# Performance work log

Hardware: AMD Instinct MI355X
Metric: run time of the kernel (lower is better)

Reference implementation:

```python
import jax, jax.numpy as jnp
import numpy as np

N0, N1, N2, N3 = 200000, 50000, 12000, 3000
E0, E1, E2 = 500000, 120000, 30000
D_IN, D_H, D_OUT = 256, 256, 64


def setup_inputs() -> dict:
    key = jax.random.key(0)
    ks = jax.random.split(key, 16)
    s = 1.0 / np.sqrt(D_IN)
    return {
        "x": jax.random.normal(ks[0], (N0, D_IN), jnp.float32),
        "src0": jax.random.randint(ks[1], (E0,), 0, N0),
        "dst0": jax.random.randint(ks[2], (E0,), 0, N1),
        "src1": jax.random.randint(ks[3], (E1,), 0, N1),
        "dst1": jax.random.randint(ks[4], (E1,), 0, N2),
        "src2": jax.random.randint(ks[5], (E2,), 0, N2),
        "dst2": jax.random.randint(ks[6], (E2,), 0, N3),
        "num_dst0": N1, "num_dst1": N2, "num_dst2": N3,
        "Ws0": jax.random.normal(ks[7], (D_IN, D_H), jnp.float32) * s,
        "Wn0": jax.random.normal(ks[8], (D_IN, D_H), jnp.float32) * s,
        "b0": jnp.zeros((D_H,), jnp.float32),
        "Ws1": jax.random.normal(ks[9], (D_H, D_H), jnp.float32) * s,
        "Wn1": jax.random.normal(ks[10], (D_H, D_H), jnp.float32) * s,
        "b1": jnp.zeros((D_H,), jnp.float32),
        "Ws2": jax.random.normal(ks[11], (D_H, D_OUT), jnp.float32) * s,
        "Wn2": jax.random.normal(ks[12], (D_H, D_OUT), jnp.float32) * s,
        "b2": jnp.zeros((D_OUT,), jnp.float32),
    }


def sage_conv(src, dst, num_dst, h_src, Wn, Ws, b):
    # DGL SAGEConv(mean): fc_self(h_dst) + fc_neigh(mean_{in-edges} h_src) + bias
    h_dst = h_src[:num_dst]
    msg = h_src[src]                                          # [E, d] gather
    agg = jax.ops.segment_sum(msg, dst, num_segments=num_dst)  # [num_dst, d]
    deg = jax.ops.segment_sum(jnp.ones((dst.shape[0],), h_src.dtype), dst,
                              num_segments=num_dst)
    h_neigh = agg / jnp.maximum(deg, 1.0)[:, None]
    return h_dst @ Ws + h_neigh @ Wn + b


def reference(x, src0, dst0, src1, dst1, src2, dst2,
              num_dst0, num_dst1, num_dst2,
              Ws0, Wn0, b0, Ws1, Wn1, b1, Ws2, Wn2, b2):
    h = sage_conv(src0, dst0, num_dst0, x, Wn0, Ws0, b0)       # layer 0 (no act, per source)
    h = sage_conv(src1, dst1, num_dst1, h, Wn1, Ws1, b1)       # layer 1
    h = jax.nn.relu(h)                                         # activation after middle layer
    # dropout omitted (eval / deterministic mode)
    h = sage_conv(src2, dst2, num_dst2, h, Wn2, Ws2, b2)       # layer 2
    return h
```

## Files before the change

### kernel.cpp

```cpp
#include <hip/hip_runtime.h>

#define N0_SRC 200000
#define N1_DST 50000
#define N2_DST 12000
#define N3_DST 3000
#define NTOT_DST 65000
#define DH 256
#define DOUT 64
#define EMAX_TOT 650000

#define CONV_BLOCKS 6250
#define TRANS_BLOCKS 1536
#define ZERO_BLOCKS 254

typedef __attribute__((ext_vector_type(8))) short short8;
typedef __attribute__((ext_vector_type(4))) float f32x4;

__device__ __forceinline__ ushort f2bf(float f) {
    union { float f; uint32_t u; } v; v.f = f;
    uint32_t r = (v.u + 0x7FFF + ((v.u >> 16) & 1)) >> 16;
    return (ushort)r;
}
__device__ __forceinline__ float bf2f(ushort u) {
    union { uint32_t u; float f; } v; v.u = ((uint32_t)u) << 16;
    return v.f;
}

__device__ __forceinline__ void gload16(const ushort* g, ushort* l) {
    __builtin_amdgcn_global_load_lds(
        (const __attribute__((address_space(1))) unsigned int*)g,
        (__attribute__((address_space(3))) unsigned int*)l,
        16, 0, 0);
}

__global__ void prep_kernel(const float* __restrict__ x,
                            const float* __restrict__ W0, const float* __restrict__ W1,
                            const float* __restrict__ W2, const float* __restrict__ W3,
                            const float* __restrict__ W4, const float* __restrict__ W5,
                            ushort* __restrict__ Wt, int* __restrict__ cnt,
                            ushort* __restrict__ xb50) {
    int bid = blockIdx.x;
    if (bid < CONV_BLOCKS) {
        long i = ((long)bid * 256 + threadIdx.x) * 8;
        float4 a = *(const float4*)(x + i);
        float4 b = *(const float4*)(x + i + 4);
        ushort4 o0, o1;
        o0.x = f2bf(a.x); o0.y = f2bf(a.y); o0.z = f2bf(a.z); o0.w = f2bf(a.w);
        o1.x = f2bf(b.x); o1.y = f2bf(b.y); o1.z = f2bf(b.z); o1.w = f2bf(b.w);
        *(ushort4*)(xb50 + i) = o0;
        *(ushort4*)(xb50 + i + 4) = o1;
        return;
    }
    if (bid < CONV_BLOCKS + TRANS_BLOCKS) {
        int tb = bid - CONV_BLOCKS;
        int wy = tb >> 8;
        int wx = tb & 255;
        const float* W; int Ndim; ushort* o;
        switch (wy) {
            case 0: W = W0; Ndim = 256; o = Wt; break;
            case 1: W = W1; Ndim = 256; o = Wt + 65536; break;
            case 2: W = W2; Ndim = 256; o = Wt + 131072; break;
            case 3: W = W3; Ndim = 256; o = Wt + 196608; break;
            case 4: W = W4; Ndim = 64;  o = Wt + 262144; break;
            default: W = W5; Ndim = 64; o = Wt + 278528; break;
        }
        int id = wx * 256 + threadIdx.x;
        int n = id >> 8;
        int k = id & 255;
        if (n >= Ndim) return;
        o[id] = f2bf(W[k * Ndim + n]);
        return;
    }
    int z = (bid - CONV_BLOCKS - TRANS_BLOCKS) * 256 + threadIdx.x;
    if (z < NTOT_DST) cnt[z] = 0;
}

__global__ void hist3_kernel(const int* __restrict__ d0, int E0,
                             const int* __restrict__ d1, int E1,
                             const int* __restrict__ d2, int E2,
                             int* __restrict__ cnt) {
    int layer = blockIdx.y;
    const int* dst; int E; int base;
    if (layer == 0)      { dst = d0; E = E0; base = 0; }
    else if (layer == 1) { dst = d1; E = E1; base = N1_DST; }
    else                 { dst = d2; E = E2; base = N1_DST + N2_DST; }
    int e = blockIdx.x * 256 + threadIdx.x;
    if (e < E) atomicAdd(&cnt[base + dst[e]], 1);
}

__global__ void fill3_kernel(const int* __restrict__ s0, const int* __restrict__ d0, int E0,
                             const int* __restrict__ s1, const int* __restrict__ d1, int E1,
                             const int* __restrict__ s2, const int* __restrict__ d2, int E2,
                             int* __restrict__ cursor, int* __restrict__ eidx) {
    int layer = blockIdx.y;
    const int* src; const int* dst; int E; int base;
    if (layer == 0)      { src = s0; dst = d0; E = E0; base = 0; }
    else if (layer == 1) { src = s1; dst = d1; E = E1; base = N1_DST; }
    else                 { src = s2; dst = d2; E = E2; base = N1_DST + N2_DST; }
    int e = blockIdx.x * 256 + threadIdx.x;
    if (e < E) {
        int p = atomicAdd(&cursor[base + dst[e]], 1);
        eidx[p] = src[e];
    }
}

__global__ void scan_phase_a(const int* __restrict__ cnt, int* __restrict__ partial, int n) {
    __shared__ int red[4];
    int t = threadIdx.x;
    int i = blockIdx.x * 1024 + t * 4;
    int s = 0;
    if (i + 3 < n) {
        int4 v = *(const int4*)(cnt + i);
        s = v.x + v.y + v.z + v.w;
    }
#pragma unroll
    for (int d = 32; d; d >>= 1) s += __shfl_down(s, d, 64);
    if ((t & 63) == 0) red[t >> 6] = s;
    __syncthreads();
    if (t == 0) partial[blockIdx.x] = red[0] + red[1] + red[2] + red[3];
}

__global__ void scan_phase_c(const int* __restrict__ cnt, const int* __restrict__ partial,
                             int* __restrict__ off, int* __restrict__ cursor, int n) {
    __shared__ int tsum[256];
    __shared__ int pbase;
    int t = threadIdx.x;
    if (t < 64) {
        int own = partial[t];
        int v = own;
#pragma unroll
        for (int d = 1; d < 64; d <<= 1) {
            int u = __shfl_up(v, d, 64);
            if (t >= d) v += u;
        }
        if (t == blockIdx.x) pbase = v - own;
    }
    int i = blockIdx.x * 1024 + t * 4;
    int4 c = make_int4(0, 0, 0, 0);
    if (i + 3 < n) c = *(const int4*)(cnt + i);
    int s = c.x + c.y + c.z + c.w;
    tsum[t] = s;
    __syncthreads();
#pragma unroll
    for (int d = 1; d < 256; d <<= 1) {
        int u = (t >= d) ? tsum[t - d] : 0;
        __syncthreads();
        tsum[t] += u;
        __syncthreads();
    }
    int base = pbase + tsum[t] - s;
    if (i + 3 < n) {
        int4 ov;
        ov.x = base;
        ov.y = ov.x + c.x;
        ov.z = ov.y + c.y;
        ov.w = ov.z + c.z;
        *(int4*)(off + i) = ov;
        *(int4*)(cursor + i) = ov;
        if (i + 4 == n) off[n] = ov.w + c.w;
    }
}

__global__ void gather_mean_f32_kernel(const float* __restrict__ h,
                                       const int* __restrict__ off,
                                       const int* __restrict__ eidx,
                                       ushort* __restrict__ hn,
                                       int num_dst) {
    int w = blockIdx.x * 4 + (threadIdx.x >> 6);
    int lane = threadIdx.x & 63;
    if (w >= num_dst) return;
    int beg = off[w];
    int end = off[w + 1];
    float a0 = 0.f, a1 = 0.f, a2 = 0.f, a3 = 0.f;
    for (int i = beg; i < end; i += 4) {
        int rem = end - i;
        int j1 = i + (rem > 1 ? 1 : 0);
        int j2 = i + (rem > 2 ? 2 : 0);
        int j3 = i + (rem > 3 ? 3 : 0);
        float m1 = rem > 1 ? 1.f : 0.f;
        float m2 = rem > 2 ? 1.f : 0.f;
        float m3 = rem > 3 ? 1.f : 0.f;
        int s0 = eidx[i], s1 = eidx[j1], s2 = eidx[j2], s3 = eidx[j3];
        float4 v0 = ((const float4*)(h + (size_t)s0 * DH))[lane];
        float4 v1 = ((const float4*)(h + (size_t)s1 * DH))[lane];
        float4 v2 = ((const float4*)(h + (size_t)s2 * DH))[lane];
        float4 v3 = ((const float4*)(h + (size_t)s3 * DH))[lane];
        a0 += v0.x + m1 * v1.x + m2 * v2.x + m3 * v3.x;
        a1 += v0.y + m1 * v1.y + m2 * v2.y + m3 * v3.y;
        a2 += v0.z + m1 * v1.z + m2 * v2.z + m3 * v3.z;
        a3 += v0.w + m1 * v1.w + m2 * v2.w + m3 * v3.w;
    }
    float inv = 1.0f / fmaxf((float)(end - beg), 1.0f);
    ushort4 o;
    o.x = f2bf(a0 * inv); o.y = f2bf(a1 * inv);
    o.z = f2bf(a2 * inv); o.w = f2bf(a3 * inv);
    *(ushort4*)(hn + (size_t)w * DH + lane * 4) = o;
}

__global__ void gather_mean_bf16_kernel(const ushort* __restrict__ h,
                                        const int* __restrict__ off,
                                        const int* __restrict__ eidx,
                                        ushort* __restrict__ hn,
                                        int num_dst) {
    int w = blockIdx.x * 4 + (threadIdx.x >> 6);
    int lane = threadIdx.x & 63;
    if (w >= num_dst) return;
    int beg = off[w];
    int end = off[w + 1];
    float a0 = 0.f, a1 = 0.f, a2 = 0.f, a3 = 0.f;
    for (int i = beg; i < end; i += 4) {
        int rem = end - i;
        int j1 = i + (rem > 1 ? 1 : 0);
        int j2 = i + (rem > 2 ? 2 : 0);
        int j3 = i + (rem > 3 ? 3 : 0);
        float m1 = rem > 1 ? 1.f : 0.f;
        float m2 = rem > 2 ? 1.f : 0.f;
        float m3 = rem > 3 ? 1.f : 0.f;
        int s0 = eidx[i], s1 = eidx[j1], s2 = eidx[j2], s3 = eidx[j3];
        ushort4 v0 = ((const ushort4*)(h + (size_t)s0 * DH))[lane];
        ushort4 v1 = ((const ushort4*)(h + (size_t)s1 * DH))[lane];
        ushort4 v2 = ((const ushort4*)(h + (size_t)s2 * DH))[lane];
        ushort4 v3 = ((const ushort4*)(h + (size_t)s3 * DH))[lane];
        a0 += bf2f(v0.x) + m1 * bf2f(v1.x) + m2 * bf2f(v2.x) + m3 * bf2f(v3.x);
        a1 += bf2f(v0.y) + m1 * bf2f(v1.y) + m2 * bf2f(v2.y) + m3 * bf2f(v3.y);
        a2 += bf2f(v0.z) + m1 * bf2f(v1.z) + m2 * bf2f(v2.z) + m3 * bf2f(v3.z);
        a3 += bf2f(v0.w) + m1 * bf2f(v1.w) + m2 * bf2f(v2.w) + m3 * bf2f(v3.w);
    }
    float inv = 1.0f / fmaxf((float)(end - beg), 1.0f);
    ushort4 o;
    o.x = f2bf(a0 * inv); o.y = f2bf(a1 * inv);
    o.z = f2bf(a2 * inv); o.w = f2bf(a3 * inv);
    *(ushort4*)(hn + (size_t)w * DH + lane * 4) = o;
}

template <int MT, int NT, bool RELU, bool OUT_BF16>
__global__ __launch_bounds__(256) void gemm_dual(const ushort* __restrict__ Ad,
                                                 const ushort* __restrict__ An,
                                                 const ushort* __restrict__ Wst,
                                                 const ushort* __restrict__ Wnt,
                                                 const float* __restrict__ bias,
                                                 void* __restrict__ Cv,
                                                 int M, int N) {
    const int K = 256;
    const int BM = MT * 64;
    const int BN = NT * 16;
    __shared__ __align__(16) ushort lds[(2 * BM + 2 * BN) * 32];
    ushort* Asd = lds;
    ushort* Asn = lds + BM * 32;
    ushort* Bss = lds + 2 * BM * 32;
    ushort* Bsn = lds + 2 * BM * 32 + BN * 32;

    int tid  = threadIdx.x;
    int lane = tid & 63;
    int wid  = tid >> 6;
    int q    = lane >> 4;
    int mr   = lane & 15;
    int row0 = blockIdx.y * BM;
    int col0 = blockIdx.x * BN;

    f32x4 acc[MT][NT];
#pragma unroll
    for (int i = 0; i < MT; ++i)
#pragma unroll
        for (int j = 0; j < NT; ++j) acc[i][j] = (f32x4){0.f, 0.f, 0.f, 0.f};

    for (int k0 = 0; k0 < K; k0 += 32) {
#pragma unroll
        for (int c = 0; c < MT; ++c) {
            int chunk = c * 256 + tid;
            int r   = chunk >> 2;
            int sg  = (chunk & 3) ^ ((r >> 1) & 3);
            int row = row0 + r;
            if (row > M - 1) row = M - 1;
            const ushort* gd = Ad + (size_t)row * K + k0 + sg * 8;
            const ushort* gn = An + (size_t)row * K + k0 + sg * 8;
            int cb = (c * 256 + (tid & ~63)) * 8;
            gload16(gd, Asd + cb);
            gload16(gn, Asn + cb);
        }
#pragma unroll
        for (int c = 0; c < NT / 4; ++c) {
            int chunk = c * 256 + tid;
            int r  = chunk >> 2;
            int sg = (chunk & 3) ^ ((r >> 1) & 3);
            const ushort* gs = Wst + (size_t)(col0 + r) * K + k0 + sg * 8;
            const ushort* gw = Wnt + (size_t)(col0 + r) * K + k0 + sg * 8;
            int cb = (c * 256 + (tid & ~63)) * 8;
            gload16(gs, Bss + cb);
            gload16(gw, Bsn + cb);
        }
        __syncthreads();

        short8 ad[MT], an[MT];
#pragma unroll
        for (int mt = 0; mt < MT; ++mt) {
            int rho = wid * (MT * 16) + mt * 16 + mr;
            int o   = rho * 32 + ((q ^ ((rho >> 1) & 3)) * 8);
            ad[mt] = *(const short8*)(Asd + o);
            an[mt] = *(const short8*)(Asn + o);
        }
#pragma unroll
        for (int nt = 0; nt < NT; ++nt) {
            int rho = nt * 16 + mr;
            int o   = rho * 32 + ((q ^ ((rho >> 1) & 3)) * 8);
            short8 bs = *(const short8*)(Bss + o);
            short8 bn = *(const short8*)(Bsn + o);
#pragma unroll
            for (int mt = 0; mt < MT; ++mt)
                acc[mt][nt] = __builtin_amdgcn_mfma_f32_16x16x32_bf16(
                    ad[mt], bs, acc[mt][nt], 0, 0, 0);
#pragma unroll
            for (int mt = 0; mt < MT; ++mt)
                acc[mt][nt] = __builtin_amdgcn_mfma_f32_16x16x32_bf16(
                    an[mt], bn, acc[mt][nt], 0, 0, 0);
        }
        __syncthreads();
    }

#pragma unroll
    for (int mt = 0; mt < MT; ++mt) {
#pragma unroll
        for (int i = 0; i < 4; ++i) {
            int row = row0 + wid * (MT * 16) + mt * 16 + q * 4 + i;
            if (row >= M) continue;
#pragma unroll
            for (int nt = 0; nt < NT; ++nt) {
                int col = col0 + nt * 16 + mr;
                float v = acc[mt][nt][i] + bias[col];
                if (RELU) v = fmaxf(v, 0.0f);
                if (OUT_BF16) ((ushort*)Cv)[(size_t)row * N + col] = f2bf(v);
                else          ((float*)Cv)[(size_t)row * N + col] = v;
            }
        }
    }
}

extern "C" void kernel_launch(void* const* d_in, const int* in_sizes, int n_in,
                              void* d_out, int out_size, void* d_ws, size_t ws_size,
                              hipStream_t stream) {
    const float* x    = (const float*)d_in[0];
    const int* src0   = (const int*)d_in[1];
    const int* dst0   = (const int*)d_in[2];
    const int* src1   = (const int*)d_in[3];
    const int* dst1   = (const int*)d_in[4];
    const int* src2   = (const int*)d_in[5];
    const int* dst2   = (const int*)d_in[6];
    const float* Ws0  = (const float*)d_in[10];
    const float* Wn0  = (const float*)d_in[11];
    const float* b0   = (const float*)d_in[12];
    const float* Ws1  = (const float*)d_in[13];
    const float* Wn1  = (const float*)d_in[14];
    const float* b1   = (const float*)d_in[15];
    const float* Ws2  = (const float*)d_in[16];
    const float* Wn2  = (const float*)d_in[17];
    const float* b2   = (const float*)d_in[18];
    float* out = (float*)d_out;

    int E0 = in_sizes[1];
    int E1 = in_sizes[3];
    int E2 = in_sizes[5];

    ushort* wsu  = (ushort*)d_ws;
    ushort* xb50 = wsu;
    ushort* hn0b = xb50 + (size_t)N1_DST * DH;
    ushort* h1b  = hn0b + (size_t)N1_DST * DH;
    ushort* hn1b = h1b  + (size_t)N1_DST * DH;
    ushort* h2b  = hn1b + (size_t)N2_DST * DH;
    ushort* hn2b = h2b  + (size_t)N2_DST * DH;
    ushort* Wt   = hn2b + (size_t)N3_DST * DH;
    ushort* Ws0t = Wt;
    ushort* Wn0t = Wt + 65536;
    ushort* Ws1t = Wt + 131072;
    ushort* Wn1t = Wt + 196608;
    ushort* Ws2t = Wt + 262144;
    ushort* Wn2t = Wt + 278528;
    int* cnt     = (int*)(Wt + 294912);
    int* off     = cnt + NTOT_DST;
    int* cursor  = off + NTOT_DST + 4;
    int* eidx    = cursor + NTOT_DST;
    int* partial = eidx + EMAX_TOT;

    prep_kernel<<<CONV_BLOCKS + TRANS_BLOCKS + ZERO_BLOCKS, 256, 0, stream>>>(
        x, Ws0, Wn0, Ws1, Wn1, Ws2, Wn2, Wt, cnt, xb50);

    int Emax = max(max(E0, E1), E2);
    int nb = (NTOT_DST + 1023) / 1024;
    hist3_kernel<<<dim3((Emax + 255) / 256, 3), 256, 0, stream>>>(dst0, E0, dst1, E1, dst2, E2, cnt);
    scan_phase_a<<<nb, 256, 0, stream>>>(cnt, partial, NTOT_DST);
    scan_phase_c<<<nb, 256, 0, stream>>>(cnt, partial, off, cursor, NTOT_DST);
    fill3_kernel<<<dim3((Emax + 255) / 256, 3), 256, 0, stream>>>(
        src0, dst0, E0, src1, dst1, E1, src2, dst2, E2, cursor, eidx);

    const int* off0 = off;
    const int* off1 = off + N1_DST;
    const int* off2 = off + N1_DST + N2_DST;

    gather_mean_f32_kernel<<<(N1_DST + 3) / 4, 256, 0, stream>>>(x, off0, eidx, hn0b, N1_DST);
    gemm_dual<2, 16, false, true><<<dim3(1, (N1_DST + 127) / 128), 256, 0, stream>>>(
        xb50, hn0b, Ws0t, Wn0t, b0, h1b, N1_DST, DH);

    gather_mean_bf16_kernel<<<(N2_DST + 3) / 4, 256, 0, stream>>>(h1b, off1, eidx, hn1b, N2_DST);
    gemm_dual<2, 16, true, true><<<dim3(1, (N2_DST + 127) / 128), 256, 0, stream>>>(
        h1b, hn1b, Ws1t, Wn1t, b1, h2b, N2_DST, DH);

    gather_mean_bf16_kernel<<<(N3_DST + 3) / 4, 256, 0, stream>>>(h2b, off2, eidx, hn2b, N3_DST);
    gemm_dual<1, 4, false, false><<<dim3(DOUT / 64, (N3_DST + 63) / 64), 256, 0, stream>>>(
        h2b, hn2b, Ws2t, Wn2t, b2, out, N3_DST, DOUT);
}
```

Measured before the change: 507.5 us.

## Fuse CSR prep into cooperative kernel, unroll gathers by eight, split GEMM tiles

The separate prep, histogram, two scan phases and fill launches become one cooperative kernel that uses grid-wide syncs between phases, which removes four launch gaps. The gather-mean kernels now issue eight row loads per iteration instead of four, giving more memory-level parallelism per wave. The layer 0 and 1 GEMMs use a 128-wide N tile over two grid columns, doubling the block count. Risks: grid.sync costs, a fixed 2048-block grid that must fit co-resident on the device, and more registers in the gather kernels.

New measurement: 1.353 ms. +166.6%, slower.

```diff
diff --git a/kernel.cpp b/kernel.cpp
--- a/kernel.cpp
+++ b/kernel.cpp
@@ -1,4 +1,7 @@
 #include <hip/hip_runtime.h>
+#include <hip/hip_cooperative_groups.h>
+
+namespace cg = cooperative_groups;
 
 #define N0_SRC 200000
 #define N1_DST 50000
@@ -9,9 +12,7 @@
 #define DOUT 64
 #define EMAX_TOT 650000
 
-#define CONV_BLOCKS 6250
-#define TRANS_BLOCKS 1536
-#define ZERO_BLOCKS 254
+#define PREP_BLOCKS 2048
 
 typedef __attribute__((ext_vector_type(8))) short short8;
 typedef __attribute__((ext_vector_type(4))) float f32x4;
@@ -33,132 +34,107 @@
         16, 0, 0);
 }
 
-__global__ void prep_kernel(const float* __restrict__ x,
-                            const float* __restrict__ W0, const float* __restrict__ W1,
-                            const float* __restrict__ W2, const float* __restrict__ W3,
-                            const float* __restrict__ W4, const float* __restrict__ W5,
-                            ushort* __restrict__ Wt, int* __restrict__ cnt,
-                            ushort* __restrict__ xb50) {
-    int bid = blockIdx.x;
-    if (bid < CONV_BLOCKS) {
-        long i = ((long)bid * 256 + threadIdx.x) * 8;
-        float4 a = *(const float4*)(x + i);
-        float4 b = *(const float4*)(x + i + 4);
-        ushort4 o0, o1;
-        o0.x = f2bf(a.x); o0.y = f2bf(a.y); o0.z = f2bf(a.z); o0.w = f2bf(a.w);
-        o1.x = f2bf(b.x); o1.y = f2bf(b.y); o1.z = f2bf(b.z); o1.w = f2bf(b.w);
-        *(ushort4*)(xb50 + i) = o0;
-        *(ushort4*)(xb50 + i + 4) = o1;
-        return;
-    }
-    if (bid < CONV_BLOCKS + TRANS_BLOCKS) {
-        int tb = bid - CONV_BLOCKS;
-        int wy = tb >> 8;
-        int wx = tb & 255;
-        const float* W; int Ndim; ushort* o;
-        switch (wy) {
-            case 0: W = W0; Ndim = 256; o = Wt; break;
-            case 1: W = W1; Ndim = 256; o = Wt + 65536; break;
-            case 2: W = W2; Ndim = 256; o = Wt + 131072; break;
-            case 3: W = W3; Ndim = 256; o = Wt + 196608; break;
-            case 4: W = W4; Ndim = 64;  o = Wt + 262144; break;
-            default: W = W5; Ndim = 64; o = Wt + 278528; break;
-        }
-        int id = wx * 256 + threadIdx.x;
-        int n = id >> 8;
-        int k = id & 255;
-        if (n >= Ndim) return;
-        o[id] = f2bf(W[k * Ndim + n]);
-        return;
-    }
-    int z = (bid - CONV_BLOCKS - TRANS_BLOCKS) * 256 + threadIdx.x;
-    if (z < NTOT_DST) cnt[z] = 0;
-}
-
-__global__ void hist3_kernel(const int* __restrict__ d0, int E0,
-                             const int* __restrict__ d1, int E1,
-                             const int* __restrict__ d2, int E2,
-                             int* __restrict__ cnt) {
-    int layer = blockIdx.y;
-    const int* dst; int E; int base;
-    if (layer == 0)      { dst = d0; E = E0; base = 0; }
-    else if (layer == 1) { dst = d1; E = E1; base = N1_DST; }
-    else                 { dst = d2; E = E2; base = N1_DST + N2_DST; }
-    int e = blockIdx.x * 256 + threadIdx.x;
-    if (e < E) atomicAdd(&cnt[base + dst[e]], 1);
-}
-
-__global__ void fill3_kernel(const int* __restrict__ s0, const int* __restrict__ d0, int E0,
-                             const int* __restrict__ s1, const int* __restrict__ d1, int E1,
-                             const int* __restrict__ s2, const int* __restrict__ d2, int E2,
-                             int* __restrict__ cursor, int* __restrict__ eidx) {
-    int layer = blockIdx.y;
-    const int* src; const int* dst; int E; int base;
-    if (layer == 0)      { src = s0; dst = d0; E = E0; base = 0; }
-    else if (layer == 1) { src = s1; dst = d1; E = E1; base = N1_DST; }
-    else                 { src = s2; dst = d2; E = E2; base = N1_DST + N2_DST; }
-    int e = blockIdx.x * 256 + threadIdx.x;
-    if (e < E) {
-        int p = atomicAdd(&cursor[base + dst[e]], 1);
-        eidx[p] = src[e];
-    }
-}
-
-__global__ void scan_phase_a(const int* __restrict__ cnt, int* __restrict__ partial, int n) {
+struct PrepArgs {
+    const float* x;
+    const float* W[6];
+    const int* s0; const int* d0; int E0;
+    const int* s1; const int* d1; int E1;
+    const int* s2; const int* d2; int E2;
+    ushort* Wt; ushort* xb50;
+    int* cnt; int* off; int* cursor; int* eidx; int* partial;
+};
+
+__global__ __launch_bounds__(256) void prep_csr_kernel(PrepArgs a) {
+    cg::grid_group grid = cg::this_grid();
     __shared__ int red[4];
-    int t = threadIdx.x;
-    int i = blockIdx.x * 1024 + t * 4;
-    int s = 0;
-    if (i + 3 < n) {
-        int4 v = *(const int4*)(cnt + i);
-        s = v.x + v.y + v.z + v.w;
-    }
-#pragma unroll
-    for (int d = 32; d; d >>= 1) s += __shfl_down(s, d, 64);
-    if ((t & 63) == 0) red[t >> 6] = s;
-    __syncthreads();
-    if (t == 0) partial[blockIdx.x] = red[0] + red[1] + red[2] + red[3];
-}
-
-__global__ void scan_phase_c(const int* __restrict__ cnt, const int* __restrict__ partial,
-                             int* __restrict__ off, int* __restrict__ cursor, int n) {
     __shared__ int tsum[256];
     __shared__ int pbase;
-    int t = threadIdx.x;
-    if (t < 64) {
-        int own = partial[t];
-        int v = own;
-#pragma unroll
-        for (int d = 1; d < 64; d <<= 1) {
-            int u = __shfl_up(v, d, 64);
-            if (t >= d) v += u;
-        }
-        if (t == blockIdx.x) pbase = v - own;
-    }
-    int i = blockIdx.x * 1024 + t * 4;
-    int4 c = make_int4(0, 0, 0, 0);
-    if (i + 3 < n) c = *(const int4*)(cnt + i);
-    int s = c.x + c.y + c.z + c.w;
-    tsum[t] = s;
-    __syncthreads();
-#pragma unroll
-    for (int d = 1; d < 256; d <<= 1) {
-        int u = (t >= d) ? tsum[t - d] : 0;
+    const int GT = PREP_BLOCKS * 256;
+    int gt = blockIdx.x * 256 + threadIdx.x;
+    int t  = threadIdx.x;
+
+    for (int i = gt; i < NTOT_DST; i += GT) a.cnt[i] = 0;
+    {
+        const float4* xv = (const float4*)a.x;
+        ushort4* xo = (ushort4*)a.xb50;
+        const int nv = N1_DST * DH / 4;
+        for (int i = gt; i < nv; i += GT) {
+            float4 v = xv[i];
+            ushort4 o;
+            o.x = f2bf(v.x); o.y = f2bf(v.y); o.z = f2bf(v.z); o.w = f2bf(v.w);
+            xo[i] = o;
+        }
+    }
+    for (int i = gt; i < 294912; i += GT) {
+        const float* W; ushort* o; int id; int Ndim;
+        if (i < 262144) { int wy = i >> 16; id = i & 65535; W = a.W[wy]; o = a.Wt + (wy << 16); Ndim = 256; }
+        else { int j = i - 262144; int wy = j >> 14; id = j & 16383; W = a.W[4 + wy]; o = a.Wt + 262144 + (wy << 14); Ndim = 64; }
+        int n = id >> 8, k = id & 255;
+        o[id] = f2bf(W[k * Ndim + n]);
+    }
+    grid.sync();
+
+    for (int e = gt; e < a.E0; e += GT) atomicAdd(&a.cnt[a.d0[e]], 1);
+    for (int e = gt; e < a.E1; e += GT) atomicAdd(&a.cnt[N1_DST + a.d1[e]], 1);
+    for (int e = gt; e < a.E2; e += GT) atomicAdd(&a.cnt[N1_DST + N2_DST + a.d2[e]], 1);
+    grid.sync();
+
+    if (blockIdx.x < 64) {
+        int i = blockIdx.x * 1024 + t * 4;
+        int s = 0;
+        if (i + 3 < NTOT_DST) {
+            int4 v = *(const int4*)(a.cnt + i);
+            s = v.x + v.y + v.z + v.w;
+        }
+#pragma unroll
+        for (int d = 32; d; d >>= 1) s += __shfl_down(s, d, 64);
+        if ((t & 63) == 0) red[t >> 6] = s;
         __syncthreads();
-        tsum[t] += u;
+        if (t == 0) a.partial[blockIdx.x] = red[0] + red[1] + red[2] + red[3];
+    }
+    grid.sync();
+
+    if (blockIdx.x < 64) {
+        if (t < 64) {
+            int own = a.partial[t];
+            int v = own;
+#pragma unroll
+            for (int d = 1; d < 64; d <<= 1) {
+                int u = __shfl_up(v, d, 64);
+                if (t >= d) v += u;
+            }
+            if (t == (int)blockIdx.x) pbase = v - own;
+        }
+        int i = blockIdx.x * 1024 + t * 4;
+        int4 c = make_int4(0, 0, 0, 0);
+        if (i + 3 < NTOT_DST) c = *(const int4*)(a.cnt + i);
+        int s = c.x + c.y + c.z + c.w;
+        tsum[t] = s;
         __syncthreads();
-    }
-    int base = pbase + tsum[t] - s;
-    if (i + 3 < n) {
-        int4 ov;
-        ov.x = base;
-        ov.y = ov.x + c.x;
-        ov.z = ov.y + c.y;
-        ov.w = ov.z + c.z;
-        *(int4*)(off + i) = ov;
-        *(int4*)(cursor + i) = ov;
-        if (i + 4 == n) off[n] = ov.w + c.w;
-    }
+#pragma unroll
+        for (int d = 1; d < 256; d <<= 1) {
+            int u = (t >= d) ? tsum[t - d] : 0;
+            __syncthreads();
+            tsum[t] += u;
+            __syncthreads();
+        }
+        int base = pbase + tsum[t] - s;
+        if (i + 3 < NTOT_DST) {
+            int4 ov;
+            ov.x = base;
+            ov.y = ov.x + c.x;
+            ov.z = ov.y + c.y;
+            ov.w = ov.z + c.z;
+            *(int4*)(a.off + i) = ov;
+            *(int4*)(a.cursor + i) = ov;
+            if (i + 4 == NTOT_DST) a.off[NTOT_DST] = ov.w + c.w;
+        }
+    }
+    grid.sync();
+
+    for (int e = gt; e < a.E0; e += GT) { int p = atomicAdd(&a.cursor[a.d0[e]], 1); a.eidx[p] = a.s0[e]; }
+    for (int e = gt; e < a.E1; e += GT) { int p = atomicAdd(&a.cursor[N1_DST + a.d1[e]], 1); a.eidx[p] = a.s1[e]; }
+    for (int e = gt; e < a.E2; e += GT) { int p = atomicAdd(&a.cursor[N1_DST + N2_DST + a.d2[e]], 1); a.eidx[p] = a.s2[e]; }
 }
 
 __global__ void gather_mean_f32_kernel(const float* __restrict__ h,
@@ -172,23 +148,40 @@
     int beg = off[w];
     int end = off[w + 1];
     float a0 = 0.f, a1 = 0.f, a2 = 0.f, a3 = 0.f;
-    for (int i = beg; i < end; i += 4) {
+    for (int i = beg; i < end; i += 8) {
         int rem = end - i;
         int j1 = i + (rem > 1 ? 1 : 0);
         int j2 = i + (rem > 2 ? 2 : 0);
         int j3 = i + (rem > 3 ? 3 : 0);
+        int j4 = i + (rem > 4 ? 4 : 0);
+        int j5 = i + (rem > 5 ? 5 : 0);
+        int j6 = i + (rem > 6 ? 6 : 0);
+        int j7 = i + (rem > 7 ? 7 : 0);
         float m1 = rem > 1 ? 1.f : 0.f;
         float m2 = rem > 2 ? 1.f : 0.f;
         float m3 = rem > 3 ? 1.f : 0.f;
-        int s0 = eidx[i], s1 = eidx[j1], s2 = eidx[j2], s3 = eidx[j3];
+        float m4 = rem > 4 ? 1.f : 0.f;
+        float m5 = rem > 5 ? 1.f : 0.f;
+        float m6 = rem > 6 ? 1.f : 0.f;
+        float m7 = rem > 7 ? 1.f : 0.f;
+        int s0 = eidx[i],  s1 = eidx[j1], s2 = eidx[j2], s3 = eidx[j3];
+        int s4 = eidx[j4], s5 = eidx[j5], s6 = eidx[j6], s7 = eidx[j7];
         float4 v0 = ((const float4*)(h + (size_t)s0 * DH))[lane];
         float4 v1 = ((const float4*)(h + (size_t)s1 * DH))[lane];
         float4 v2 = ((const float4*)(h + (size_t)s2 * DH))[lane];
         float4 v3 = ((const float4*)(h + (size_t)s3 * DH))[lane];
-        a0 += v0.x + m1 * v1.x + m2 * v2.x + m3 * v3.x;
-        a1 += v0.y + m1 * v1.y + m2 * v2.y + m3 * v3.y;
-        a2 += v0.z + m1 * v1.z + m2 * v2.z + m3 * v3.z;
-        a3 += v0.w + m1 * v1.w + m2 * v2.w + m3 * v3.w;
+        float4 v4 = ((const float4*)(h + (size_t)s4 * DH))[lane];
+        float4 v5 = ((const float4*)(h + (size_t)s5 * DH))[lane];
+        float4 v6 = ((const float4*)(h + (size_t)s6 * DH))[lane];
+        float4 v7 = ((const float4*)(h + (size_t)s7 * DH))[lane];
+        a0 += (v0.x + m1 * v1.x + m2 * v2.x + m3 * v3.x) +
+              (m4 * v4.x + m5 * v5.x + m6 * v6.x + m7 * v7.x);
+        a1 += (v0.y + m1 * v1.y + m2 * v2.y + m3 * v3.y) +
+              (m4 * v4.y + m5 * v5.y + m6 * v6.y + m7 * v7.y);
+        a2 += (v0.z + m1 * v1.z + m2 * v2.z + m3 * v3.z) +
+              (m4 * v4.z + m5 * v5.z + m6 * v6.z + m7 * v7.z);
+        a3 += (v0.w + m1 * v1.w + m2 * v2.w + m3 * v3.w) +
+              (m4 * v4.w + m5 * v5.w + m6 * v6.w + m7 * v7.w);
     }
     float inv = 1.0f / fmaxf((float)(end - beg), 1.0f);
     ushort4 o;
@@ -208,23 +201,40 @@
     int beg = off[w];
     int end = off[w + 1];
     float a0 = 0.f, a1 = 0.f, a2 = 0.f, a3 = 0.f;
-    for (int i = beg; i < end; i += 4) {
+    for (int i = beg; i < end; i += 8) {
         int rem = end - i;
         int j1 = i + (rem > 1 ? 1 : 0);
         int j2 = i + (rem > 2 ? 2 : 0);
         int j3 = i + (rem > 3 ? 3 : 0);
+        int j4 = i + (rem > 4 ? 4 : 0);
+        int j5 = i + (rem > 5 ? 5 : 0);
+        int j6 = i + (rem > 6 ? 6 : 0);
+        int j7 = i + (rem > 7 ? 7 : 0);
         float m1 = rem > 1 ? 1.f : 0.f;
         float m2 = rem > 2 ? 1.f : 0.f;
         float m3 = rem > 3 ? 1.f : 0.f;
-        int s0 = eidx[i], s1 = eidx[j1], s2 = eidx[j2], s3 = eidx[j3];
+        float m4 = rem > 4 ? 1.f : 0.f;
+        float m5 = rem > 5 ? 1.f : 0.f;
+        float m6 = rem > 6 ? 1.f : 0.f;
+        float m7 = rem > 7 ? 1.f : 0.f;
+        int s0 = eidx[i],  s1 = eidx[j1], s2 = eidx[j2], s3 = eidx[j3];
+        int s4 = eidx[j4], s5 = eidx[j5], s6 = eidx[j6], s7 = eidx[j7];
         ushort4 v0 = ((const ushort4*)(h + (size_t)s0 * DH))[lane];
         ushort4 v1 = ((const ushort4*)(h + (size_t)s1 * DH))[lane];
         ushort4 v2 = ((const ushort4*)(h + (size_t)s2 * DH))[lane];
         ushort4 v3 = ((const ushort4*)(h + (size_t)s3 * DH))[lane];
-        a0 += bf2f(v0.x) + m1 * bf2f(v1.x) + m2 * bf2f(v2.x) + m3 * bf2f(v3.x);
-        a1 += bf2f(v0.y) + m1 * bf2f(v1.y) + m2 * bf2f(v2.y) + m3 * bf2f(v3.y);
-        a2 += bf2f(v0.z) + m1 * bf2f(v1.z) + m2 * bf2f(v2.z) + m3 * bf2f(v3.z);
-        a3 += bf2f(v0.w) + m1 * bf2f(v1.w) + m2 * bf2f(v2.w) + m3 * bf2f(v3.w);
+        ushort4 v4 = ((const ushort4*)(h + (size_t)s4 * DH))[lane];
+        ushort4 v5 = ((const ushort4*)(h + (size_t)s5 * DH))[lane];
+        ushort4 v6 = ((const ushort4*)(h + (size_t)s6 * DH))[lane];
+        ushort4 v7 = ((const ushort4*)(h + (size_t)s7 * DH))[lane];
+        a0 += (bf2f(v0.x) + m1 * bf2f(v1.x) + m2 * bf2f(v2.x) + m3 * bf2f(v3.x)) +
+              (m4 * bf2f(v4.x) + m5 * bf2f(v5.x) + m6 * bf2f(v6.x) + m7 * bf2f(v7.x));
+        a1 += (bf2f(v0.y) + m1 * bf2f(v1.y) + m2 * bf2f(v2.y) + m3 * bf2f(v3.y)) +
+              (m4 * bf2f(v4.y) + m5 * bf2f(v5.y) + m6 * bf2f(v6.y) + m7 * bf2f(v7.y));
+        a2 += (bf2f(v0.z) + m1 * bf2f(v1.z) + m2 * bf2f(v2.z) + m3 * bf2f(v3.z)) +
+              (m4 * bf2f(v4.z) + m5 * bf2f(v5.z) + m6 * bf2f(v6.z) + m7 * bf2f(v7.z));
+        a3 += (bf2f(v0.w) + m1 * bf2f(v1.w) + m2 * bf2f(v2.w) + m3 * bf2f(v3.w)) +
+              (m4 * bf2f(v4.w) + m5 * bf2f(v5.w) + m6 * bf2f(v6.w) + m7 * bf2f(v7.w));
     }
     float inv = 1.0f / fmaxf((float)(end - beg), 1.0f);
     ushort4 o;
@@ -380,27 +390,30 @@
     int* eidx    = cursor + NTOT_DST;
     int* partial = eidx + EMAX_TOT;
 
-    prep_kernel<<<CONV_BLOCKS + TRANS_BLOCKS + ZERO_BLOCKS, 256, 0, stream>>>(
-        x, Ws0, Wn0, Ws1, Wn1, Ws2, Wn2, Wt, cnt, xb50);
-
-    int Emax = max(max(E0, E1), E2);
-    int nb = (NTOT_DST + 1023) / 1024;
-    hist3_kernel<<<dim3((Emax + 255) / 256, 3), 256, 0, stream>>>(dst0, E0, dst1, E1, dst2, E2, cnt);
-    scan_phase_a<<<nb, 256, 0, stream>>>(cnt, partial, NTOT_DST);
-    scan_phase_c<<<nb, 256, 0, stream>>>(cnt, partial, off, cursor, NTOT_DST);
-    fill3_kernel<<<dim3((Emax + 255) / 256, 3), 256, 0, stream>>>(
-        src0, dst0, E0, src1, dst1, E1, src2, dst2, E2, cursor, eidx);
+    PrepArgs pa;
+    pa.x = x;
+    pa.W[0] = Ws0; pa.W[1] = Wn0; pa.W[2] = Ws1;
+    pa.W[3] = Wn1; pa.W[4] = Ws2; pa.W[5] = Wn2;
+    pa.s0 = src0; pa.d0 = dst0; pa.E0 = E0;
+    pa.s1 = src1; pa.d1 = dst1; pa.E1 = E1;
+    pa.s2 = src2; pa.d2 = dst2; pa.E2 = E2;
+    pa.Wt = Wt; pa.xb50 = xb50;
+    pa.cnt = cnt; pa.off = off; pa.cursor = cursor;
+    pa.eidx = eidx; pa.partial = partial;
+    void* kargs[] = { &pa };
+    hipLaunchCooperativeKernel((void*)prep_csr_kernel, dim3(PREP_BLOCKS), dim3(256),
+                               kargs, 0, stream);
 
     const int* off0 = off;
     const int* off1 = off + N1_DST;
     const int* off2 = off + N1_DST + N2_DST;
 
     gather_mean_f32_kernel<<<(N1_DST + 3) / 4, 256, 0, stream>>>(x, off0, eidx, hn0b, N1_DST);
-    gemm_dual<2, 16, false, true><<<dim3(1, (N1_DST + 127) / 128), 256, 0, stream>>>(
+    gemm_dual<2, 8, false, true><<<dim3(DH / 128, (N1_DST + 127) / 128), 256, 0, stream>>>(
         xb50, hn0b, Ws0t, Wn0t, b0, h1b, N1_DST, DH);
 
     gather_mean_bf16_kernel<<<(N2_DST + 3) / 4, 256, 0, stream>>>(h1b, off1, eidx, hn1b, N2_DST);
-    gemm_dual<2, 16, true, true><<<dim3(1, (N2_DST + 127) / 128), 256, 0, stream>>>(
+    gemm_dual<2, 8, true, true><<<dim3(DH / 128, (N2_DST + 127) / 128), 256, 0, stream>>>(
         h1b, hn1b, Ws1t, Wn1t, b1, h2b, N2_DST, DH);
 
     gather_mean_bf16_kernel<<<(N3_DST + 3) / 4, 256, 0, stream>>>(h2b, off2, eidx, hn2b, N3_DST);
```
